# Optimization experiments

Hardware: AMD Instinct MI355X
Metric: run time of the kernel (lower is better)

The kernel has to match this reference:

```python
import jax, jax.numpy as jnp
import numpy as np

L = 32            # num_layers
R = 16            # lora_rank
P = L * 7         # 224 projections
D = 256           # encoder d_model
H = 4             # encoder heads
HD = D // H
FF = 2048         # TransformerEncoderLayer default dim_feedforward
PED = 512         # proj_embed_dim
HID = 4096
KV = 8 * (4096 // 32)   # 1024
INTER = 11008
VOCAB = 50000
NEG = -1e9

# projection index groups within the P=7*L ordering [q,k,v,o,gate,up,down]
IDX_A_HID = jnp.asarray((np.arange(L)[:, None] * 7 + np.array([0, 1, 2, 3, 4, 5])).reshape(-1))  # in_dim=4096
IDX_A_INT = jnp.asarray(np.arange(L) * 7 + 6)                                                    # in_dim=11008
IDX_B_HID = jnp.asarray((np.arange(L)[:, None] * 7 + np.array([0, 3, 6])).reshape(-1))           # out_dim=4096
IDX_B_KV  = jnp.asarray((np.arange(L)[:, None] * 7 + np.array([1, 2])).reshape(-1))              # out_dim=1024
IDX_B_INT = jnp.asarray((np.arange(L)[:, None] * 7 + np.array([4, 5])).reshape(-1))              # out_dim=11008


def _ln(x, g, b, eps=1e-5):
    m = jnp.mean(x, -1, keepdims=True)
    v = jnp.mean((x - m) ** 2, -1, keepdims=True)
    return (x - m) * jax.lax.rsqrt(v + eps) * g + b


def _enc_layer(x, pad, qw, qb, ow, ob, g1, b1, f1w, f1b, f2w, f2b, g2, b2):
    # post-norm TransformerEncoderLayer (torch default), relu FFN, eval mode (no dropout)
    Bsz, S, _ = x.shape
    qkv = x @ qw.T + qb                                  # [B,S,3D]
    q, k, v = jnp.split(qkv, 3, axis=-1)
    hd = lambda t: t.reshape(Bsz, S, H, HD).transpose(0, 2, 1, 3)
    q, k, v = hd(q), hd(k), hd(v)
    s = jnp.einsum('bhqd,bhkd->bhqk', q, k) / jnp.asarray(np.sqrt(HD), x.dtype)
    s = jnp.where(pad[:, None, None, :], NEG, s)
    a = jax.nn.softmax(s, -1)
    o = jnp.einsum('bhqk,bhkd->bhqd', a, v).transpose(0, 2, 1, 3).reshape(Bsz, S, D)
    x = _ln(x + o @ ow.T + ob, g1, b1)
    f = jax.nn.relu(x @ f1w.T + f1b) @ f2w.T + f2b
    return _ln(x + f, g2, b2)


def _forward(condition_ids, attention_mask, embed_table, enc_qkv_w, enc_qkv_b, enc_out_w, enc_out_b,
             enc_ln1_g, enc_ln1_b, enc_ff1_w, enc_ff1_b, enc_ff2_w, enc_ff2_b, enc_ln2_g, enc_ln2_b,
             proj_w, proj_b, a1_w, a1_b, a2_w, a2_b, b1_w, b1_b, b2_w, b2_b, scales):
    Bsz = condition_ids.shape[0]
    x = embed_table[condition_ids]                       # [B,S,256]
    pad = attention_mask == 0                            # key padding mask (~attention_mask)
    for l in range(3):
        x = _enc_layer(x, pad, enc_qkv_w[l], enc_qkv_b[l], enc_out_w[l], enc_out_b[l],
                       enc_ln1_g[l], enc_ln1_b[l], enc_ff1_w[l], enc_ff1_b[l],
                       enc_ff2_w[l], enc_ff2_b[l], enc_ln2_g[l], enc_ln2_b[l])
    am = attention_mask.astype(x.dtype)
    pooled = (x * am[..., None]).sum(1) / jnp.clip(am.sum(1, keepdims=True), 1.0)   # masked mean pool
    pe = (pooled @ proj_w.T + proj_b).reshape(Bsz, P, PED)                          # [B,224,512]

    def dec(w1, b1_, w2, b2_):
        return jax.nn.gelu(pe @ w1.T + b1_, approximate=False) @ w2.T + b2_

    A_base = dec(a1_w, a1_b, a2_w, a2_b).reshape(Bsz, P, R, 64)   # [B,P,r,64]
    B_base = dec(b1_w, b1_b, b2_w, b2_b).reshape(Bsz, P, 64, R)   # [B,P,64,r]
    sa, sb = scales[:, 0], scales[:, 1]

    def tile_A(idx, in_d):
        # all in_dims divisible by 64 => repeat(in_d//64+1)[:, :in_d] == exact tiling
        a = A_base[:, idx] * sa[idx][None, :, None, None]
        return jnp.tile(a, (1, 1, 1, in_d // 64))

    def tile_B(idx, out_d):
        b = B_base[:, idx] * sb[idx][None, :, None, None]
        return jnp.tile(b, (1, 1, out_d // 64, 1))

    return (tile_A(IDX_A_HID, HID), tile_A(IDX_A_INT, INTER),
            tile_B(IDX_B_HID, HID), tile_B(IDX_B_KV, KV), tile_B(IDX_B_INT, INTER))


def setup_inputs() -> dict:
    key = jax.random.key(0)
    ks = iter(jax.random.split(key, 40))
    rn = lambda shape, s=0.02: jax.random.normal(next(ks), shape, jnp.float32) * s
    Bsz, S = 4, 128
    return {
        'condition_ids': jax.random.randint(next(ks), (Bsz, S), 0, VOCAB),
        'attention_mask': jnp.ones((Bsz, S), jnp.int32),
        'embed_table': rn((VOCAB, D)),
        'enc_qkv_w': rn((3, 3 * D, D)), 'enc_qkv_b': rn((3, 3 * D)),
        'enc_out_w': rn((3, D, D)), 'enc_out_b': rn((3, D)),
        'enc_ln1_g': jnp.ones((3, D)), 'enc_ln1_b': jnp.zeros((3, D)),
        'enc_ff1_w': rn((3, FF, D)), 'enc_ff1_b': rn((3, FF)),
        'enc_ff2_w': rn((3, D, FF)), 'enc_ff2_b': rn((3, D)),
        'enc_ln2_g': jnp.ones((3, D)), 'enc_ln2_b': jnp.zeros((3, D)),
        'proj_w': rn((P * PED, D)), 'proj_b': rn((P * PED,)),
        'a1_w': rn((D, PED)), 'a1_b': rn((D,)),
        'a2_w': rn((R * 64, D)), 'a2_b': rn((R * 64,)),
        'b1_w': rn((D, PED)), 'b1_b': rn((D,)),
        'b2_w': rn((R * 64, D)), 'b2_b': rn((R * 64,)),
        'scales': jnp.full((P, 2), 0.01, jnp.float32),
    }


def reference(condition_ids, attention_mask, embed_table, enc_qkv_w, enc_qkv_b, enc_out_w, enc_out_b,
              enc_ln1_g, enc_ln1_b, enc_ff1_w, enc_ff1_b, enc_ff2_w, enc_ff2_b, enc_ln2_g, enc_ln2_b,
              proj_w, proj_b, a1_w, a1_b, a2_w, a2_b, b1_w, b1_b, b2_w, b2_b, scales):
    return _forward(condition_ids, attention_mask, embed_table, enc_qkv_w, enc_qkv_b, enc_out_w, enc_out_b,
                    enc_ln1_g, enc_ln1_b, enc_ff1_w, enc_ff1_b, enc_ff2_w, enc_ff2_b, enc_ln2_g, enc_ln2_b,
                    proj_w, proj_b, a1_w, a1_b, a2_w, a2_b, b1_w, b1_b, b2_w, b2_b, scales)
```

## Files before the change

### kernel.cpp

```cpp
#include <hip/hip_runtime.h>
#include <hip/hip_bf16.h>

typedef unsigned short u16;
typedef unsigned int u32;

__global__ void embed_kernel(const int* __restrict__ ids, const float* __restrict__ emb,
                             float* __restrict__ x) {
  int tok = blockIdx.x, d = threadIdx.x;
  x[tok * 256 + d] = emb[(size_t)ids[tok] * 256 + d];
}

template <int ACT>
__global__ __launch_bounds__(256) void gemm_kernel(const float* __restrict__ A,
    const float* __restrict__ W, const float* __restrict__ bias, float* __restrict__ C,
    int M, int N, int K) {
  __shared__ float As[16][68];
  __shared__ float Ws[16][68];
  const int t = threadIdx.x;
  const int m0 = blockIdx.x * 64, n0 = blockIdx.y * 64;
  const int tn = t & 15, tm = t >> 4;
  const int lr = t >> 2, lk = (t & 3) * 4;
  float acc[4][4] = {};
  for (int k0 = 0; k0 < K; k0 += 16) {
    float4 av = *(const float4*)(A + (size_t)(m0 + lr) * K + k0 + lk);
    float4 wv = *(const float4*)(W + (size_t)(n0 + lr) * K + k0 + lk);
    As[lk + 0][lr] = av.x; As[lk + 1][lr] = av.y; As[lk + 2][lr] = av.z; As[lk + 3][lr] = av.w;
    Ws[lk + 0][lr] = wv.x; Ws[lk + 1][lr] = wv.y; Ws[lk + 2][lr] = wv.z; Ws[lk + 3][lr] = wv.w;
    __syncthreads();
#pragma unroll
    for (int kk = 0; kk < 16; ++kk) {
      float4 a = *(const float4*)&As[kk][tm * 4];
      float4 w4 = *(const float4*)&Ws[kk][tn * 4];
      acc[0][0] += a.x * w4.x; acc[0][1] += a.x * w4.y; acc[0][2] += a.x * w4.z; acc[0][3] += a.x * w4.w;
      acc[1][0] += a.y * w4.x; acc[1][1] += a.y * w4.y; acc[1][2] += a.y * w4.z; acc[1][3] += a.y * w4.w;
      acc[2][0] += a.z * w4.x; acc[2][1] += a.z * w4.y; acc[2][2] += a.z * w4.z; acc[2][3] += a.z * w4.w;
      acc[3][0] += a.w * w4.x; acc[3][1] += a.w * w4.y; acc[3][2] += a.w * w4.z; acc[3][3] += a.w * w4.w;
    }
    __syncthreads();
  }
#pragma unroll
  for (int i = 0; i < 4; ++i) {
    int row = m0 + tm * 4 + i;
    float4 o;
    float* po = (float*)&o;
#pragma unroll
    for (int j = 0; j < 4; ++j) {
      int col = n0 + tn * 4 + j;
      float v = acc[i][j] + bias[col];
      if (ACT == 1) v = fmaxf(v, 0.f);
      if (ACT == 2) v = 0.5f * v * (1.f + erff(v * 0.70710678118654752f));
      po[j] = v;
    }
    *(float4*)(C + (size_t)row * N + n0 + tn * 4) = o;
  }
}

__global__ __launch_bounds__(256) void gemm_part_kernel(const float* __restrict__ A,
    const float* __restrict__ W, float* __restrict__ Cpart, int M, int N, int K, int KS) {
  __shared__ float As[16][68];
  __shared__ float Ws[16][68];
  const int t = threadIdx.x;
  const int m0 = blockIdx.x * 64, n0 = blockIdx.y * 64;
  const int kz = blockIdx.z;
  const int tn = t & 15, tm = t >> 4;
  const int lr = t >> 2, lk = (t & 3) * 4;
  float acc[4][4] = {};
  const int kend = kz * KS + KS;
  for (int k0 = kz * KS; k0 < kend; k0 += 16) {
    float4 av = *(const float4*)(A + (size_t)(m0 + lr) * K + k0 + lk);
    float4 wv = *(const float4*)(W + (size_t)(n0 + lr) * K + k0 + lk);
    As[lk + 0][lr] = av.x; As[lk + 1][lr] = av.y; As[lk + 2][lr] = av.z; As[lk + 3][lr] = av.w;
    Ws[lk + 0][lr] = wv.x; Ws[lk + 1][lr] = wv.y; Ws[lk + 2][lr] = wv.z; Ws[lk + 3][lr] = wv.w;
    __syncthreads();
#pragma unroll
    for (int kk = 0; kk < 16; ++kk) {
      float4 a = *(const float4*)&As[kk][tm * 4];
      float4 w4 = *(const float4*)&Ws[kk][tn * 4];
      acc[0][0] += a.x * w4.x; acc[0][1] += a.x * w4.y; acc[0][2] += a.x * w4.z; acc[0][3] += a.x * w4.w;
      acc[1][0] += a.y * w4.x; acc[1][1] += a.y * w4.y; acc[1][2] += a.y * w4.z; acc[1][3] += a.y * w4.w;
      acc[2][0] += a.z * w4.x; acc[2][1] += a.z * w4.y; acc[2][2] += a.z * w4.z; acc[2][3] += a.z * w4.w;
      acc[3][0] += a.w * w4.x; acc[3][1] += a.w * w4.y; acc[3][2] += a.w * w4.z; acc[3][3] += a.w * w4.w;
    }
    __syncthreads();
  }
  float* Cz = Cpart + (size_t)kz * M * N;
#pragma unroll
  for (int i = 0; i < 4; ++i) {
    int row = m0 + tm * 4 + i;
    float4 o;
    o.x = acc[i][0]; o.y = acc[i][1]; o.z = acc[i][2]; o.w = acc[i][3];
    *(float4*)(Cz + (size_t)row * N + n0 + tn * 4) = o;
  }
}

template <int ACT>
__global__ void red_bias_act_kernel(const float* __restrict__ parts, int nparts, int pstride,
                                    const float* __restrict__ bias, float* __restrict__ dst, int N) {
  int idx = blockIdx.x * 256 + threadIdx.x;
  float v = bias[idx % N];
  for (int p = 0; p < nparts; ++p) v += parts[(size_t)p * pstride + idx];
  if (ACT == 1) v = fmaxf(v, 0.f);
  if (ACT == 2) v = 0.5f * v * (1.f + erff(v * 0.70710678118654752f));
  dst[idx] = v;
}

__global__ __launch_bounds__(256) void attn_kernel(const float* __restrict__ qkv,
    const int* __restrict__ mask, float* __restrict__ o) {
  __shared__ float Klds[8192];
  __shared__ float Vlds[8192];
  const int blk = blockIdx.x;
  const int b = blk >> 7, h = (blk >> 5) & 3, qg = blk & 31;
  const int t = threadIdx.x;
  for (int i = t; i < 8192; i += 256) {
    int s = i >> 6, d = i & 63;
    size_t base = (size_t)(b * 128 + s) * 768 + h * 64 + d;
    Klds[(s << 6) + (d ^ (s & 31))] = qkv[base + 256];
    Vlds[i] = qkv[base + 512];
  }
  __syncthreads();
  const int wave = t >> 6, lane = t & 63;
  const int q = qg * 4 + wave;
  float qv = qkv[(size_t)(b * 128 + q) * 768 + h * 64 + lane];
  const int m0i = mask[b * 128 + lane];
  const int m1i = mask[b * 128 + 64 + lane];
  float s0 = 0.f, s1 = 0.f;
  const int sw = lane & 31;
  for (int d = 0; d < 64; ++d) {
    float qd = __shfl(qv, d);
    s0 += qd * Klds[(lane << 6) + (d ^ sw)];
    s1 += qd * Klds[((lane + 64) << 6) + (d ^ sw)];
  }
  s0 *= 0.125f; s1 *= 0.125f;
  if (m0i == 0) s0 = -1000000000.0f;
  if (m1i == 0) s1 = -1000000000.0f;
  float m = fmaxf(s0, s1);
  for (int off = 32; off; off >>= 1) m = fmaxf(m, __shfl_xor(m, off));
  float p0 = expf(s0 - m), p1 = expf(s1 - m);
  float sum = p0 + p1;
  for (int off = 32; off; off >>= 1) sum += __shfl_xor(sum, off);
  float rs = 1.f / sum;
  float acc = 0.f;
  for (int k = 0; k < 64; ++k) acc += __shfl(p0, k) * Vlds[(k << 6) + lane];
  for (int k = 0; k < 64; ++k) acc += __shfl(p1, k) * Vlds[((k + 64) << 6) + lane];
  o[(size_t)(b * 128 + q) * 256 + h * 64 + lane] = acc * rs;
}

__global__ __launch_bounds__(256) void add_ln_red_kernel(float* __restrict__ x,
    const float* __restrict__ parts, int nparts, int pstride, const float* __restrict__ bias,
    const float* __restrict__ g, const float* __restrict__ b) {
  int tok = blockIdx.x, t = threadIdx.x;
  int idx = tok * 256 + t;
  float r = x[idx] + bias[t];
  for (int p = 0; p < nparts; ++p) r += parts[(size_t)p * pstride + idx];
  float s = r, sq = r * r;
  for (int off = 32; off; off >>= 1) { s += __shfl_xor(s, off); sq += __shfl_xor(sq, off); }
  __shared__ float red[8];
  int wave = t >> 6, lane = t & 63;
  if (lane == 0) { red[wave] = s; red[4 + wave] = sq; }
  __syncthreads();
  float S = red[0] + red[1] + red[2] + red[3];
  float SQ = red[4] + red[5] + red[6] + red[7];
  float mean = S * (1.f / 256.f);
  float var = SQ * (1.f / 256.f) - mean * mean;
  float inv = 1.f / sqrtf(fmaxf(var, 0.f) + 1e-5f);
  x[idx] = (r - mean) * inv * g[t] + b[t];
}

__global__ void pool_kernel(const float* __restrict__ x, const int* __restrict__ mask,
                            float* __restrict__ pooled) {
  int b = blockIdx.x, d = threadIdx.x;
  float s = 0.f, c = 0.f;
  for (int ss = 0; ss < 128; ++ss) {
    float m = (float)mask[b * 128 + ss];
    s += m * x[(size_t)(b * 128 + ss) * 256 + d];
    c += m;
  }
  pooled[b * 256 + d] = s / fmaxf(c, 1.f);
}

__global__ __launch_bounds__(256) void proj_kernel(const float* __restrict__ pooled,
    const float* __restrict__ W, const float* __restrict__ bias, float* __restrict__ pe) {
  __shared__ float pl[1024];
  int t = threadIdx.x;
  for (int i = t; i < 1024; i += 256) pl[i] = pooled[i];
  __syncthreads();
  int wave = t >> 6, lane = t & 63;
  int half = lane >> 5, sl = lane & 31;
  int row = blockIdx.x * 8 + wave * 2 + half;
  float4 w0 = *(const float4*)(W + (size_t)row * 256 + sl * 8);
  float4 w1 = *(const float4*)(W + (size_t)row * 256 + sl * 8 + 4);
  float a0, a1, a2, a3;
#pragma unroll
  for (int bb = 0; bb < 4; ++bb) {
    const float* pp = &pl[bb * 256 + sl * 8];
    float v = w0.x * pp[0] + w0.y * pp[1] + w0.z * pp[2] + w0.w * pp[3]
            + w1.x * pp[4] + w1.y * pp[5] + w1.z * pp[6] + w1.w * pp[7];
    if (bb == 0) a0 = v; else if (bb == 1) a1 = v; else if (bb == 2) a2 = v; else a3 = v;
  }
#pragma unroll
  for (int off = 1; off < 32; off <<= 1) {
    a0 += __shfl_xor(a0, off); a1 += __shfl_xor(a1, off);
    a2 += __shfl_xor(a2, off); a3 += __shfl_xor(a3, off);
  }
  if (sl == 0) {
    float bv = bias[row];
    pe[0 * 114688 + row] = a0 + bv;
    pe[1 * 114688 + row] = a1 + bv;
    pe[2 * 114688 + row] = a2 + bv;
    pe[3 * 114688 + row] = a3 + bv;
  }
}

__global__ __launch_bounds__(256) void tile_a_kernel(const float* __restrict__ Abase,
    const float* __restrict__ scales, float* __restrict__ out, int nI, int ind,
    int pdiv, int pmul, int padd) {
  int row = blockIdx.x;
  int r = row & 15, bi = row >> 4;
  int i = bi % nI, b = bi / nI;
  int p = (i / pdiv) * 7 + (i % pdiv) * pmul + padd;
  float s = scales[2 * p];
  __shared__ float chunk[64];
  int t = threadIdx.x;
  if (t < 64) chunk[t] = Abase[((size_t)(b * 224 + p) * 16 + r) * 64 + t] * s;
  __syncthreads();
  size_t ob = (size_t)row * ind;
  for (int u = t; u * 4 < ind; u += 256) {
    int c0 = u * 4;
    float4 ov = *(const float4*)&chunk[c0 & 63];
    *(float4*)(out + ob + c0) = ov;
  }
}

__global__ __launch_bounds__(256) void tile_b_kernel(const float* __restrict__ Bbase,
    const float* __restrict__ scales, float* __restrict__ out, int nI, int ind, int nchunks,
    int pdiv, int pmul, int padd) {
  int blk = blockIdx.x;
  int cc = blk % nchunks, bi = blk / nchunks;
  int i = bi % nI, b = bi / nI;
  int p = (i / pdiv) * 7 + (i % pdiv) * pmul + padd;
  float s = scales[2 * p + 1];
  __shared__ float chunk[1024];
  int t = threadIdx.x;
  for (int e = t; e < 1024; e += 256) chunk[e] = Bbase[(size_t)(b * 224 + p) * 1024 + e] * s;
  __syncthreads();
  int cchunk16 = (ind / nchunks) * 16;
  size_t ob = (size_t)bi * ind * 16 + (size_t)cc * cchunk16;
  for (int u = t; u * 4 < cchunk16; u += 256) {
    int e0 = u * 4;
    int cabs = (cc * cchunk16 + e0) >> 4;
    int src = ((cabs & 63) << 4) + (e0 & 15);
    float4 ov = *(const float4*)&chunk[src];
    *(float4*)(out + ob + e0) = ov;
  }
}

extern "C" void kernel_launch(void* const* d_in, const int* in_sizes, int n_in,
                              void* d_out, int out_size, void* d_ws, size_t ws_size,
                              hipStream_t stream) {
  const int* ids     = (const int*)d_in[0];
  const int* mask    = (const int*)d_in[1];
  const float* emb   = (const float*)d_in[2];
  const float* qkv_w = (const float*)d_in[3];
  const float* qkv_b = (const float*)d_in[4];
  const float* out_w = (const float*)d_in[5];
  const float* out_b = (const float*)d_in[6];
  const float* ln1_g = (const float*)d_in[7];
  const float* ln1_b = (const float*)d_in[8];
  const float* ff1_w = (const float*)d_in[9];
  const float* ff1_b = (const float*)d_in[10];
  const float* ff2_w = (const float*)d_in[11];
  const float* ff2_b = (const float*)d_in[12];
  const float* ln2_g = (const float*)d_in[13];
  const float* ln2_b = (const float*)d_in[14];
  const float* proj_w = (const float*)d_in[15];
  const float* proj_b = (const float*)d_in[16];
  const float* a1_w = (const float*)d_in[17];
  const float* a1_b = (const float*)d_in[18];
  const float* a2_w = (const float*)d_in[19];
  const float* a2_b = (const float*)d_in[20];
  const float* b1_w = (const float*)d_in[21];
  const float* b1_b = (const float*)d_in[22];
  const float* b2_w = (const float*)d_in[23];
  const float* b2_b = (const float*)d_in[24];
  const float* scales = (const float*)d_in[25];

  float* w = (float*)d_ws;
  float* x      = w + 0;
  float* qkv    = w + 262144;
  float* attn_o = w + 655360;
  float* ff     = w + 786432;
  float* pooled = w + 1835008;
  float* pe     = w + 1836032;
  float* hA     = w + 2294784;
  float* hB     = w + 2524160;
  float* Abase  = w + 2753536;
  float* Bbase  = w + 3671040;
  float* parts  = w + 4588544;

  float* out = (float*)d_out;

  embed_kernel<<<512, 256, 0, stream>>>(ids, emb, x);
  for (int l = 0; l < 3; ++l) {
    gemm_kernel<0><<<dim3(8, 12), 256, 0, stream>>>(x, qkv_w + l * 768 * 256, qkv_b + l * 768,
                                                    qkv, 512, 768, 256);
    attn_kernel<<<512, 256, 0, stream>>>(qkv, mask, attn_o);
    gemm_part_kernel<<<dim3(8, 4, 4), 256, 0, stream>>>(attn_o, out_w + l * 256 * 256, parts,
                                                        512, 256, 256, 64);
    add_ln_red_kernel<<<512, 256, 0, stream>>>(x, parts, 4, 131072, out_b + l * 256,
                                               ln1_g + l * 256, ln1_b + l * 256);
    gemm_kernel<1><<<dim3(8, 32), 256, 0, stream>>>(x, ff1_w + l * 2048 * 256, ff1_b + l * 2048,
                                                    ff, 512, 2048, 256);
    gemm_part_kernel<<<dim3(8, 4, 8), 256, 0, stream>>>(ff, ff2_w + l * 256 * 2048, parts,
                                                        512, 256, 2048, 256);
    add_ln_red_kernel<<<512, 256, 0, stream>>>(x, parts, 8, 131072, ff2_b + l * 256,
                                               ln2_g + l * 256, ln2_b + l * 256);
  }
  pool_kernel<<<4, 256, 0, stream>>>(x, mask, pooled);
  proj_kernel<<<14336, 256, 0, stream>>>(pooled, proj_w, proj_b, pe);

  gemm_part_kernel<<<dim3(14, 4, 4), 256, 0, stream>>>(pe, a1_w, parts, 896, 256, 512, 128);
  red_bias_act_kernel<2><<<896, 256, 0, stream>>>(parts, 4, 229376, a1_b, hA, 256);
  gemm_kernel<0><<<dim3(14, 16), 256, 0, stream>>>(hA, a2_w, a2_b, Abase, 896, 1024, 256);

  gemm_part_kernel<<<dim3(14, 4, 4), 256, 0, stream>>>(pe, b1_w, parts, 896, 256, 512, 128);
  red_bias_act_kernel<2><<<896, 256, 0, stream>>>(parts, 4, 229376, b1_b, hB, 256);
  gemm_kernel<0><<<dim3(14, 16), 256, 0, stream>>>(hB, b2_w, b2_b, Bbase, 896, 1024, 256);

  tile_a_kernel<<<12288, 256, 0, stream>>>(Abase, scales, out, 192, 4096, 6, 1, 0);
  tile_a_kernel<<<2048, 256, 0, stream>>>(Abase, scales, out + 50331648ull, 32, 11008, 1, 0, 6);
  tile_b_kernel<<<3072, 256, 0, stream>>>(Bbase, scales, out + 72876032ull, 96, 4096, 8, 3, 3, 0);
  tile_b_kernel<<<512, 256, 0, stream>>>(Bbase, scales, out + 98041856ull, 64, 1024, 2, 2, 1, 1);
  tile_b_kernel<<<2048, 256, 0, stream>>>(Bbase, scales, out + 102236160ull, 64, 11008, 8, 2, 1, 4);
}
```

Measured before the change: 1.056 ms.

## Replace FP32 SIMT GEMMs with bf16 MFMA GEMM kernel

Merges the full-K and split-K FP32 GEMM kernels into one templated kernel that converts fp32 tiles to bf16 in shared memory and runs the 16x16x32 bf16 MFMA instruction. It is meant to cut the FMA-bound cost of the encoder and LoRA-generator GEMMs. Rounding inputs to bf16 loses precision against the fp32 reference. The output tiles are 64x64 with 32-deep K steps.

```diff
diff --git a/kernel.cpp b/kernel.cpp
--- a/kernel.cpp
+++ b/kernel.cpp
@@ -3,6 +3,17 @@
 
 typedef unsigned short u16;
 typedef unsigned int u32;
+typedef __attribute__((ext_vector_type(8))) short short8;
+typedef __attribute__((ext_vector_type(4))) float floatx4;
+
+__device__ __forceinline__ u16 f2bf(float f) {
+  u32 x = __float_as_uint(f);
+  x += 0x7FFFu + ((x >> 16) & 1u);
+  return (u16)(x >> 16);
+}
+__device__ __forceinline__ u32 pk2(float lo, float hi) {
+  return (u32)f2bf(lo) | ((u32)f2bf(hi) << 16);
+}
 
 __global__ void embed_kernel(const int* __restrict__ ids, const float* __restrict__ emb,
                              float* __restrict__ x) {
@@ -10,86 +21,62 @@
   x[tok * 256 + d] = emb[(size_t)ids[tok] * 256 + d];
 }
 
-template <int ACT>
-__global__ __launch_bounds__(256) void gemm_kernel(const float* __restrict__ A,
+template <int ACT, int SPLIT>
+__global__ __launch_bounds__(256) void mfma_gemm_kernel(const float* __restrict__ A,
     const float* __restrict__ W, const float* __restrict__ bias, float* __restrict__ C,
-    int M, int N, int K) {
-  __shared__ float As[16][68];
-  __shared__ float Ws[16][68];
-  const int t = threadIdx.x;
-  const int m0 = blockIdx.x * 64, n0 = blockIdx.y * 64;
-  const int tn = t & 15, tm = t >> 4;
-  const int lr = t >> 2, lk = (t & 3) * 4;
-  float acc[4][4] = {};
-  for (int k0 = 0; k0 < K; k0 += 16) {
-    float4 av = *(const float4*)(A + (size_t)(m0 + lr) * K + k0 + lk);
-    float4 wv = *(const float4*)(W + (size_t)(n0 + lr) * K + k0 + lk);
-    As[lk + 0][lr] = av.x; As[lk + 1][lr] = av.y; As[lk + 2][lr] = av.z; As[lk + 3][lr] = av.w;
-    Ws[lk + 0][lr] = wv.x; Ws[lk + 1][lr] = wv.y; Ws[lk + 2][lr] = wv.z; Ws[lk + 3][lr] = wv.w;
-    __syncthreads();
-#pragma unroll
-    for (int kk = 0; kk < 16; ++kk) {
-      float4 a = *(const float4*)&As[kk][tm * 4];
-      float4 w4 = *(const float4*)&Ws[kk][tn * 4];
-      acc[0][0] += a.x * w4.x; acc[0][1] += a.x * w4.y; acc[0][2] += a.x * w4.z; acc[0][3] += a.x * w4.w;
-      acc[1][0] += a.y * w4.x; acc[1][1] += a.y * w4.y; acc[1][2] += a.y * w4.z; acc[1][3] += a.y * w4.w;
-      acc[2][0] += a.z * w4.x; acc[2][1] += a.z * w4.y; acc[2][2] += a.z * w4.z; acc[2][3] += a.z * w4.w;
-      acc[3][0] += a.w * w4.x; acc[3][1] += a.w * w4.y; acc[3][2] += a.w * w4.z; acc[3][3] += a.w * w4.w;
-    }
-    __syncthreads();
-  }
-#pragma unroll
-  for (int i = 0; i < 4; ++i) {
-    int row = m0 + tm * 4 + i;
-    float4 o;
-    float* po = (float*)&o;
-#pragma unroll
-    for (int j = 0; j < 4; ++j) {
-      int col = n0 + tn * 4 + j;
-      float v = acc[i][j] + bias[col];
-      if (ACT == 1) v = fmaxf(v, 0.f);
-      if (ACT == 2) v = 0.5f * v * (1.f + erff(v * 0.70710678118654752f));
-      po[j] = v;
-    }
-    *(float4*)(C + (size_t)row * N + n0 + tn * 4) = o;
-  }
-}
-
-__global__ __launch_bounds__(256) void gemm_part_kernel(const float* __restrict__ A,
-    const float* __restrict__ W, float* __restrict__ Cpart, int M, int N, int K, int KS) {
-  __shared__ float As[16][68];
-  __shared__ float Ws[16][68];
+    int M, int N, int K, int KS, int pstride) {
+  __shared__ u16 Abf[64 * 32];
+  __shared__ u16 Wbf[64 * 32];
   const int t = threadIdx.x;
   const int m0 = blockIdx.x * 64, n0 = blockIdx.y * 64;
   const int kz = blockIdx.z;
-  const int tn = t & 15, tm = t >> 4;
-  const int lr = t >> 2, lk = (t & 3) * 4;
-  float acc[4][4] = {};
-  const int kend = kz * KS + KS;
-  for (int k0 = kz * KS; k0 < kend; k0 += 16) {
-    float4 av = *(const float4*)(A + (size_t)(m0 + lr) * K + k0 + lk);
-    float4 wv = *(const float4*)(W + (size_t)(n0 + lr) * K + k0 + lk);
-    As[lk + 0][lr] = av.x; As[lk + 1][lr] = av.y; As[lk + 2][lr] = av.z; As[lk + 3][lr] = av.w;
-    Ws[lk + 0][lr] = wv.x; Ws[lk + 1][lr] = wv.y; Ws[lk + 2][lr] = wv.z; Ws[lk + 3][lr] = wv.w;
+  const int srow = t >> 2, skc = (t & 3) * 8;
+  const int w = t >> 6, lane = t & 63;
+  const int q = lane >> 4, rr = lane & 15;
+  floatx4 acc[4];
+#pragma unroll
+  for (int i = 0; i < 4; ++i) acc[i] = (floatx4){0.f, 0.f, 0.f, 0.f};
+
+  const int kbeg = kz * KS, kend = kbeg + KS;
+  for (int k0 = kbeg; k0 < kend; k0 += 32) {
+    const float* ga = A + (size_t)(m0 + srow) * K + k0 + skc;
+    const float* gw = W + (size_t)(n0 + srow) * K + k0 + skc;
+    float4 a0 = *(const float4*)ga;
+    float4 a1 = *(const float4*)(ga + 4);
+    float4 w0 = *(const float4*)gw;
+    float4 w1 = *(const float4*)(gw + 4);
+    uint4 pa, pw;
+    pa.x = pk2(a0.x, a0.y); pa.y = pk2(a0.z, a0.w);
+    pa.z = pk2(a1.x, a1.y); pa.w = pk2(a1.z, a1.w);
+    pw.x = pk2(w0.x, w0.y); pw.y = pk2(w0.z, w0.w);
+    pw.z = pk2(w1.x, w1.y); pw.w = pk2(w1.z, w1.w);
     __syncthreads();
-#pragma unroll
-    for (int kk = 0; kk < 16; ++kk) {
-      float4 a = *(const float4*)&As[kk][tm * 4];
-      float4 w4 = *(const float4*)&Ws[kk][tn * 4];
-      acc[0][0] += a.x * w4.x; acc[0][1] += a.x * w4.y; acc[0][2] += a.x * w4.z; acc[0][3] += a.x * w4.w;
-      acc[1][0] += a.y * w4.x; acc[1][1] += a.y * w4.y; acc[1][2] += a.y * w4.z; acc[1][3] += a.y * w4.w;
-      acc[2][0] += a.z * w4.x; acc[2][1] += a.z * w4.y; acc[2][2] += a.z * w4.z; acc[2][3] += a.z * w4.w;
-      acc[3][0] += a.w * w4.x; acc[3][1] += a.w * w4.y; acc[3][2] += a.w * w4.z; acc[3][3] += a.w * w4.w;
+    *(uint4*)&Abf[srow * 32 + skc] = pa;
+    *(uint4*)&Wbf[srow * 32 + skc] = pw;
+    __syncthreads();
+    short8 af = *(short8*)&Abf[(w * 16 + rr) * 32 + q * 8];
+#pragma unroll
+    for (int ct = 0; ct < 4; ++ct) {
+      short8 bf = *(short8*)&Wbf[(ct * 16 + rr) * 32 + q * 8];
+      acc[ct] = __builtin_amdgcn_mfma_f32_16x16x32_bf16(af, bf, acc[ct], 0, 0, 0);
     }
-    __syncthreads();
-  }
-  float* Cz = Cpart + (size_t)kz * M * N;
-#pragma unroll
-  for (int i = 0; i < 4; ++i) {
-    int row = m0 + tm * 4 + i;
-    float4 o;
-    o.x = acc[i][0]; o.y = acc[i][1]; o.z = acc[i][2]; o.w = acc[i][3];
-    *(float4*)(Cz + (size_t)row * N + n0 + tn * 4) = o;
+  }
+
+  float* dst = SPLIT ? (C + (size_t)kz * pstride) : C;
+#pragma unroll
+  for (int ct = 0; ct < 4; ++ct) {
+    int col = n0 + ct * 16 + rr;
+#pragma unroll
+    for (int r = 0; r < 4; ++r) {
+      int row = m0 + w * 16 + q * 4 + r;
+      float v = acc[ct][r];
+      if (!SPLIT) {
+        v += bias[col];
+        if (ACT == 1) v = fmaxf(v, 0.f);
+        if (ACT == 2) v = 0.5f * v * (1.f + erff(v * 0.70710678118654752f));
+      }
+      dst[(size_t)row * N + col] = v;
+    }
   }
 }
 
@@ -301,30 +288,34 @@
 
   embed_kernel<<<512, 256, 0, stream>>>(ids, emb, x);
   for (int l = 0; l < 3; ++l) {
-    gemm_kernel<0><<<dim3(8, 12), 256, 0, stream>>>(x, qkv_w + l * 768 * 256, qkv_b + l * 768,
-                                                    qkv, 512, 768, 256);
+    mfma_gemm_kernel<0, 0><<<dim3(8, 12), 256, 0, stream>>>(
+        x, qkv_w + l * 768 * 256, qkv_b + l * 768, qkv, 512, 768, 256, 256, 0);
     attn_kernel<<<512, 256, 0, stream>>>(qkv, mask, attn_o);
-    gemm_part_kernel<<<dim3(8, 4, 4), 256, 0, stream>>>(attn_o, out_w + l * 256 * 256, parts,
-                                                        512, 256, 256, 64);
+    mfma_gemm_kernel<0, 1><<<dim3(8, 4, 4), 256, 0, stream>>>(
+        attn_o, out_w + l * 256 * 256, nullptr, parts, 512, 256, 256, 64, 131072);
     add_ln_red_kernel<<<512, 256, 0, stream>>>(x, parts, 4, 131072, out_b + l * 256,
                                                ln1_g + l * 256, ln1_b + l * 256);
-    gemm_kernel<1><<<dim3(8, 32), 256, 0, stream>>>(x, ff1_w + l * 2048 * 256, ff1_b + l * 2048,
-                                                    ff, 512, 2048, 256);
-    gemm_part_kernel<<<dim3(8, 4, 8), 256, 0, stream>>>(ff, ff2_w + l * 256 * 2048, parts,
-                                                        512, 256, 2048, 256);
+    mfma_gemm_kernel<1, 0><<<dim3(8, 32), 256, 0, stream>>>(
+        x, ff1_w + l * 2048 * 256, ff1_b + l * 2048, ff, 512, 2048, 256, 256, 0);
+    mfma_gemm_kernel<0, 1><<<dim3(8, 4, 8), 256, 0, stream>>>(
+        ff, ff2_w + l * 256 * 2048, nullptr, parts, 512, 256, 2048, 256, 131072);
     add_ln_red_kernel<<<512, 256, 0, stream>>>(x, parts, 8, 131072, ff2_b + l * 256,
                                                ln2_g + l * 256, ln2_b + l * 256);
   }
   pool_kernel<<<4, 256, 0, stream>>>(x, mask, pooled);
   proj_kernel<<<14336, 256, 0, stream>>>(pooled, proj_w, proj_b, pe);
 
-  gemm_part_kernel<<<dim3(14, 4, 4), 256, 0, stream>>>(pe, a1_w, parts, 896, 256, 512, 128);
+  mfma_gemm_kernel<0, 1><<<dim3(14, 4, 4), 256, 0, stream>>>(
+      pe, a1_w, nullptr, parts, 896, 256, 512, 128, 229376);
   red_bias_act_kernel<2><<<896, 256, 0, stream>>>(parts, 4, 229376, a1_b, hA, 256);
-  gemm_kernel<0><<<dim3(14, 16), 256, 0, stream>>>(hA, a2_w, a2_b, Abase, 896, 1024, 256);
-
-  gemm_part_kernel<<<dim3(14, 4, 4), 256, 0, stream>>>(pe, b1_w, parts, 896, 256, 512, 128);
+  mfma_gemm_kernel<0, 0><<<dim3(14, 16), 256, 0, stream>>>(
+      hA, a2_w, a2_b, Abase, 896, 1024, 256, 256, 0);
+
+  mfma_gemm_kernel<0, 1><<<dim3(14, 4, 4), 256, 0, stream>>>(
+      pe, b1_w, nullptr, parts, 896, 256, 512, 128, 229376);
   red_bias_act_kernel<2><<<896, 256, 0, stream>>>(parts, 4, 229376, b1_b, hB, 256);
-  gemm_kernel<0><<<dim3(14, 16), 256, 0, stream>>>(hB, b2_w, b2_b, Bbase, 896, 1024, 256);
+  mfma_gemm_kernel<0, 0><<<dim3(14, 16), 256, 0, stream>>>(
+      hB, b2_w, b2_b, Bbase, 896, 1024, 256, 256, 0);
 
   tile_a_kernel<<<12288, 256, 0, stream>>>(Abase, scales, out, 192, 4096, 6, 1, 0);
   tile_a_kernel<<<2048, 256, 0, stream>>>(Abase, scales, out + 50331648ull, 32, 11008, 1, 0, 6);
```

Measured after the change: 974.3 us. -7.7%, faster.
